# Optimization experiments

Measured on AMD Instinct MI355X. Metric: run time of the kernel, lower is better.

The kernel has to match this reference:

```python
import jax, jax.numpy as jnp
import numpy as np

B, C, D = 2, 2048, 1024   # batch, seq_len, hidden_size
I = 2048                  # intermediate_size (GLU hidden)
E, K = 8, 2               # n_experts, top_k
CF = 1.25                 # capacity factor


def setup_inputs() -> dict:
    key = jax.random.key(0)
    k1, k2, k3, k4 = jax.random.split(key, 4)
    scale = 0.02
    return {
        "hidden_states": jax.random.normal(k1, (B, C, D), jnp.float32),
        "Wg": jax.random.normal(k2, (E, D), jnp.float32) * scale,      # router gate weight [E, d]
        "W1": jax.random.normal(k3, (E, D, 2 * I), jnp.float32) * scale,  # expert in-proj
        "W2": jax.random.normal(k4, (E, I, D), jnp.float32) * scale,      # expert out-proj
    }


def reference(hidden_states, Wg, W1, W2):
    Bx, Cx, d = hidden_states.shape
    N = Bx * Cx
    cap = int(N * K * CF / E)  # exp_capacity (static)
    x = hidden_states.reshape(N, d)

    # --- router (eval mode: no noise) ---
    logits = x @ Wg.T                          # [N, E]
    top_v, top_i = jax.lax.top_k(logits, K)    # [N, K]
    gates = jax.nn.softmax(top_v, axis=-1)     # [N, K]

    # --- greedy capacity-limited assignment (token-major, then k), vectorized ---
    flat_e = top_i.reshape(N * K)              # expert id per (token, k) slot, in loop order
    gates_f = gates.reshape(N * K)
    tok = jnp.repeat(jnp.arange(N), K)         # token id per slot
    onehot = jax.nn.one_hot(flat_e, E, dtype=jnp.int32)
    pos = jnp.cumsum(onehot, axis=0) - 1       # running count per expert
    pos_f = jnp.take_along_axis(pos, flat_e[:, None], axis=1)[:, 0]
    keep = pos_f < cap                         # slots beyond capacity are dropped
    pos_safe = jnp.where(keep, pos_f, cap)     # out-of-range -> dropped by mode='drop'

    # --- dispatch: exp_batches[e, pos] = x[token] ---
    exp_batches = jnp.zeros((E, cap, d), x.dtype).at[flat_e, pos_safe].set(x[tok], mode='drop')

    # --- per-expert GLU MLP (batched over experts) ---
    h = jnp.einsum('ecd,edf->ecf', exp_batches, W1)       # [E, cap, 2I]
    inp, gate = jnp.split(h, 2, axis=-1)
    h = jax.nn.gelu(inp, approximate=False) * gate        # exact gelu, matches torch
    exp_out = jnp.einsum('eci,eid->ecd', h, W2)           # [E, cap, d]

    # --- combine: equals exp_mask.view(N,-1) @ exp_out.view(-1,d) ---
    gathered = exp_out[flat_e, jnp.minimum(pos_safe, cap - 1)]  # [N*K, d]
    contrib = jnp.where(keep, gates_f, 0.0)[:, None] * gathered
    out = jax.ops.segment_sum(contrib, tok, num_segments=N)    # [N, d]
    return out.reshape(Bx, Cx, d)
```

## Files before the change

kernel.cpp:

```cpp
#include <hip/hip_runtime.h>
#include <hip/hip_bf16.h>
#include <math.h>

#define N_TOK 4096
#define DIM   1024
#define NEXP  8
#define IDIM  2048
#define TWOI  4096
#define CAP   1280

#define W1_BLOCKS (64 * 16 * NEXP)
#define W2_BLOCKS (16 * 32 * NEXP)
#define ROUTER_BLOCKS (N_TOK / 4)

#define G1X 32
#define G1Y 10
#define G1_TRANS_Z ((W2_BLOCKS + G1X * G1Y - 1) / (G1X * G1Y))

using short8  = __attribute__((ext_vector_type(8))) short;
using floatx4 = __attribute__((ext_vector_type(4))) float;

__device__ __forceinline__ unsigned short f2b(float f) {
  __hip_bfloat16 h = __float2bfloat16(f);
  return *reinterpret_cast<unsigned short*>(&h);
}

__device__ __forceinline__ void async16(const unsigned short* g, unsigned short* l) {
  __builtin_amdgcn_global_load_lds(
      (const __attribute__((address_space(1))) unsigned int*)g,
      (__attribute__((address_space(3))) unsigned int*)l,
      16, 0, 0);
}

__device__ __forceinline__ void block_barrier() {
  __builtin_amdgcn_sched_barrier(0);
  asm volatile("" ::: "memory");
  __builtin_amdgcn_s_barrier();
  asm volatile("" ::: "memory");
  __builtin_amdgcn_sched_barrier(0);
}

__global__ __launch_bounds__(256) void prologue_kernel(const float* __restrict__ W1,
                                                       unsigned short* __restrict__ w1t,
                                                       const float* __restrict__ x,
                                                       const float* __restrict__ Wg,
                                                       unsigned short* __restrict__ xb,
                                                       int* __restrict__ top_i,
                                                       float* __restrict__ gates) {
  __shared__ __align__(16) float smem_f[NEXP * DIM];
  int bid = blockIdx.x;
  int tid = threadIdx.x;

  if (bid < W1_BLOCKS) {
    float (*tile)[65] = reinterpret_cast<float (*)[65]>(smem_f);
    int e = bid >> 10;
    int t = bid & 1023;
    const int R = DIM, C = TWOI;
    int r0 = (t & 15) * 64;
    int c0 = (t >> 4) * 64;
    const float* s = W1 + (size_t)e * R * C;
    unsigned short* d = w1t + (size_t)e * R * C;
    int tr = tid >> 4, tc = (tid & 15) * 4;
#pragma unroll
    for (int i = 0; i < 4; i++) {
      float4 v = *reinterpret_cast<const float4*>(&s[(size_t)(r0 + tr + i * 16) * C + c0 + tc]);
      tile[tr + i * 16][tc]     = v.x;
      tile[tr + i * 16][tc + 1] = v.y;
      tile[tr + i * 16][tc + 2] = v.z;
      tile[tr + i * 16][tc + 3] = v.w;
    }
    __syncthreads();
#pragma unroll
    for (int j = 0; j < 4; j++) {
      int c = (tid >> 4) + j * 16;
      int r4 = (tid & 15) * 4;
      ushort4 o;
      o.x = f2b(tile[r4][c]);
      o.y = f2b(tile[r4 + 1][c]);
      o.z = f2b(tile[r4 + 2][c]);
      o.w = f2b(tile[r4 + 3][c]);
      *reinterpret_cast<ushort4*>(&d[(size_t)(c0 + c) * R + r0 + r4]) = o;
    }
  } else {
    int rb = bid - W1_BLOCKS;
    float* wg = smem_f;
    for (int i = tid * 4; i < NEXP * DIM; i += 256 * 4) {
      *reinterpret_cast<float4*>(wg + i) = *reinterpret_cast<const float4*>(Wg + i);
    }
    __syncthreads();
    int wave = tid >> 6, lane = tid & 63;
    int t = rb * 4 + wave;
    const float* xr = x + (size_t)t * DIM;
    unsigned short* xbr = xb + (size_t)t * DIM;
    double acc[NEXP];
#pragma unroll
    for (int e = 0; e < NEXP; e++) acc[e] = 0.0;
    for (int i = lane; i < DIM; i += 64) {
      float xf = xr[i];
      xbr[i] = f2b(xf);
      double xv = (double)xf;
#pragma unroll
      for (int e = 0; e < NEXP; e++) acc[e] += xv * (double)wg[e * DIM + i];
    }
#pragma unroll
    for (int e = 0; e < NEXP; e++) {
#pragma unroll
      for (int m = 1; m < 64; m <<= 1) acc[e] += __shfl_xor(acc[e], m, 64);
    }
    if (lane == 0) {
      int i0 = 0; double v0 = acc[0];
      for (int e = 1; e < NEXP; e++) { if (acc[e] > v0) { v0 = acc[e]; i0 = e; } }
      int i1 = -1; double v1 = -1e300;
      for (int e = 0; e < NEXP; e++) { if (e != i0 && acc[e] > v1) { v1 = acc[e]; i1 = e; } }
      double e1 = exp(v1 - v0);
      float g0 = (float)(1.0 / (1.0 + e1));
      float g1 = (float)(e1 / (1.0 + e1));
      top_i[t * 2] = i0; top_i[t * 2 + 1] = i1;
      gates[t * 2] = g0; gates[t * 2 + 1] = g1;
    }
  }
}

__global__ __launch_bounds__(1024) void scan_kernel(const int* __restrict__ top_i,
                                                    const float* __restrict__ gates,
                                                    int* __restrict__ rowtok,
                                                    int* __restrict__ rowslot,
                                                    float* __restrict__ rowgate,
                                                    float* __restrict__ tokgate,
                                                    int* __restrict__ cnt) {
  __shared__ int hist[NEXP][1024];
  int t = threadIdx.x;
  int s0 = t * 8;
  int eloc[8];
  int c[NEXP];
#pragma unroll
  for (int e = 0; e < NEXP; e++) c[e] = 0;
#pragma unroll
  for (int j = 0; j < 8; j++) { int e = top_i[s0 + j]; eloc[j] = e; c[e]++; }
#pragma unroll
  for (int e = 0; e < NEXP; e++) hist[e][t] = c[e];
  __syncthreads();
  for (int step = 1; step < 1024; step <<= 1) {
    int tmp[NEXP];
#pragma unroll
    for (int e = 0; e < NEXP; e++) tmp[e] = (t >= step) ? hist[e][t - step] : 0;
    __syncthreads();
#pragma unroll
    for (int e = 0; e < NEXP; e++) hist[e][t] += tmp[e];
    __syncthreads();
  }
  int base[NEXP];
#pragma unroll
  for (int e = 0; e < NEXP; e++) base[e] = hist[e][t] - c[e];
  if (t < NEXP) {
    int tot = hist[t][1023];
    cnt[t] = tot < CAP ? tot : CAP;
  }
#pragma unroll
  for (int j = 0; j < 8; j++) {
    int s = s0 + j;
    int e = eloc[j];
    int pos = base[e]++;
    bool keep = pos < CAP;
    tokgate[s] = keep ? gates[s] : 0.0f;
    if (keep) {
      rowtok[e * CAP + pos]  = s >> 1;
      rowslot[e * CAP + pos] = s & 1;
      rowgate[e * CAP + pos] = gates[s];
    }
  }
}

__global__ __launch_bounds__(256, 2) void gemm1_kernel(const unsigned short* __restrict__ xb,
                                                       const unsigned short* __restrict__ w1t,
                                                       const int* __restrict__ rowtok,
                                                       const int* __restrict__ cnt,
                                                       unsigned short* __restrict__ H,
                                                       const float* __restrict__ W2,
                                                       unsigned short* __restrict__ w2t) {
  __shared__ __align__(16) unsigned char smem[65536];
  int tid  = threadIdx.x;
  int z = blockIdx.z;

  if (z >= NEXP) {
    int id = (z - NEXP) * (G1X * G1Y) + blockIdx.y * G1X + blockIdx.x;
    if (id >= W2_BLOCKS) return;
    float (*tile)[65] = reinterpret_cast<float (*)[65]>(smem);
    int e = id >> 9;
    int t = id & 511;
    const int R = IDIM, C = DIM;
    int r0 = (t & 31) * 64;
    int c0 = (t >> 5) * 64;
    const float* s = W2 + (size_t)e * R * C;
    unsigned short* d = w2t + (size_t)e * R * C;
    int tr = tid >> 4, tc = (tid & 15) * 4;
#pragma unroll
    for (int i = 0; i < 4; i++) {
      float4 v = *reinterpret_cast<const float4*>(&s[(size_t)(r0 + tr + i * 16) * C + c0 + tc]);
      tile[tr + i * 16][tc]     = v.x;
      tile[tr + i * 16][tc + 1] = v.y;
      tile[tr + i * 16][tc + 2] = v.z;
      tile[tr + i * 16][tc + 3] = v.w;
    }
    __syncthreads();
#pragma unroll
    for (int j = 0; j < 4; j++) {
      int c = (tid >> 4) + j * 16;
      int r4 = (tid & 15) * 4;
      ushort4 o;
      o.x = f2b(tile[r4][c]);
      o.y = f2b(tile[r4 + 1][c]);
      o.z = f2b(tile[r4 + 2][c]);
      o.w = f2b(tile[r4 + 3][c]);
      *reinterpret_cast<ushort4*>(&d[(size_t)(c0 + c) * R + r0 + r4]) = o;
    }
    return;
  }

  int e  = z;
  int m0 = blockIdx.y * 128;
  int i0 = blockIdx.x * 64;
  int cnte = cnt[e];
  if (m0 >= cnte) return;

  int lane = tid & 63;
  int wave = tid >> 6;

  int srA0 = wave * 32 + (lane >> 2);
  int srA1 = srA0 + 16;
  int srB  = wave * 16 + (lane >> 2);
  int sk   = (lane & 3) * 8;

  int ma0 = m0 + srA0, ma1 = m0 + srA1;
  int tok0 = (ma0 < cnte) ? rowtok[e * CAP + ma0] : 0;
  int tok1 = (ma1 < cnte) ? rowtok[e * CAP + ma1] : 0;

  const unsigned short* w1e = w1t + (size_t)e * TWOI * DIM;
  const unsigned short* gA0 = xb + (size_t)tok0 * DIM + sk;
  const unsigned short* gA1 = xb + (size_t)tok1 * DIM + sk;
  const unsigned short* gBi = w1e + (size_t)(i0 + srB) * DIM + sk;
  const unsigned short* gBg = w1e + (size_t)(i0 + srB + IDIM) * DIM + sk;

  int lane16 = lane & 15;
  int quad   = lane >> 4;
  int wm = (wave & 1) * 64;
  int wn = (wave >> 1) * 32;

  auto stage = [&](int s, int k0) {
#pragma unroll
    for (int b = 0; b < 2; b++) {
      int kk = k0 + b * 32;
      unsigned short* A  = (unsigned short*)(smem + s * 32768 + b * 8192);
      unsigned short* Bi = (unsigned short*)(smem + s * 32768 + 16384 + b * 4096);
      unsigned short* Bg = (unsigned short*)(smem + s * 32768 + 24576 + b * 4096);
      async16(gA0 + kk, A + (wave * 2 + 0) * 512);
      async16(gA1 + kk, A + (wave * 2 + 1) * 512);
      async16(gBi + kk, Bi + wave * 512);
      async16(gBg + kk, Bg + wave * 512);
    }
  };

  floatx4 acc_i[4][2], acc_g[4][2];
#pragma unroll
  for (int i = 0; i < 4; i++)
#pragma unroll
    for (int j = 0; j < 2; j++) {
      acc_i[i][j] = (floatx4){0.f, 0.f, 0.f, 0.f};
      acc_g[i][j] = (floatx4){0.f, 0.f, 0.f, 0.f};
    }

  const int T = DIM / 64;
  stage(0, 0);
  stage(1, 64);
  for (int t = 0; t < T; ++t) {
    if (t < T - 1) asm volatile("s_waitcnt vmcnt(8)" ::: "memory");
    else           asm volatile("s_waitcnt vmcnt(0)" ::: "memory");
    block_barrier();

    int s = t & 1;
#pragma unroll
    for (int b = 0; b < 2; b++) {
      const unsigned short* Ab  = (const unsigned short*)(smem + s * 32768 + b * 8192);
      const unsigned short* Bib = (const unsigned short*)(smem + s * 32768 + 16384 + b * 4096);
      const unsigned short* Bgb = (const unsigned short*)(smem + s * 32768 + 24576 + b * 4096);
      short8 a[4];
#pragma unroll
      for (int i = 0; i < 4; i++)
        a[i] = *(const short8*)&Ab[(wm + i * 16 + lane16) * 32 + quad * 8];
#pragma unroll
      for (int j = 0; j < 2; j++) {
        short8 bi = *(const short8*)&Bib[(wn + j * 16 + lane16) * 32 + quad * 8];
#pragma unroll
        for (int i = 0; i < 4; i++)
          acc_i[i][j] = __builtin_amdgcn_mfma_f32_16x16x32_bf16(a[i], bi, acc_i[i][j], 0, 0, 0);
        short8 bg = *(const short8*)&Bgb[(wn + j * 16 + lane16) * 32 + quad * 8];
#pragma unroll
        for (int i = 0; i < 4; i++)
          acc_g[i][j] = __builtin_amdgcn_mfma_f32_16x16x32_bf16(a[i], bg, acc_g[i][j], 0, 0, 0);
      }
    }

    block_barrier();
    if (t + 2 < T) stage(s, (t + 2) * 64);
  }

  unsigned short* He = H + (size_t)e * CAP * IDIM;
#pragma unroll
  for (int i = 0; i < 4; i++) {
#pragma unroll
    for (int r = 0; r < 4; r++) {
      int m = m0 + wm + i * 16 + quad * 4 + r;
#pragma unroll
      for (int j = 0; j < 2; j++) {
        int n = i0 + wn + j * 16 + lane16;
        float vi = acc_i[i][j][r];
        float vg = acc_g[i][j][r];
        float h = 0.5f * vi * (1.0f + erff(vi * 0.70710678118654752f)) * vg;
        He[(size_t)m * IDIM + n] = f2b(h);
      }
    }
  }
}

__global__ __launch_bounds__(256, 2) void gemm2_kernel(const unsigned short* __restrict__ H,
                                                       const unsigned short* __restrict__ w2t,
                                                       const int* __restrict__ cnt,
                                                       const int* __restrict__ rowtok,
                                                       const int* __restrict__ rowslot,
                                                       const float* __restrict__ rowgate,
                                                       float* __restrict__ out2) {
  int e  = blockIdx.z;
  int m0 = blockIdx.y * 128;
  int n0 = blockIdx.x * 128;
  int cnte = cnt[e];
  if (m0 >= cnte) return;

  __shared__ __align__(16) unsigned char smem[65536];

  int tid  = threadIdx.x;
  int lane = tid & 63;
  int wave = tid >> 6;

  int sr0 = wave * 32 + (lane >> 2);
  int sr1 = sr0 + 16;
  int sk  = (lane & 3) * 8;

  const unsigned short* He  = H + (size_t)e * CAP * IDIM;
  const unsigned short* w2e = w2t + (size_t)e * DIM * IDIM;
  const unsigned short* gA0 = He + (size_t)(m0 + sr0) * IDIM + sk;
  const unsigned short* gA1 = He + (size_t)(m0 + sr1) * IDIM + sk;
  const unsigned short* gB0 = w2e + (size_t)(n0 + sr0) * IDIM + sk;
  const unsigned short* gB1 = w2e + (size_t)(n0 + sr1) * IDIM + sk;

  int lane16 = lane & 15;
  int quad   = lane >> 4;
  int wm = (wave & 1) * 64;
  int wn = (wave >> 1) * 64;

  auto stage = [&](int s, int k0) {
#pragma unroll
    for (int b = 0; b < 2; b++) {
      int kk = k0 + b * 32;
      unsigned short* A = (unsigned short*)(smem + s * 32768 + b * 8192);
      unsigned short* B = (unsigned short*)(smem + s * 32768 + 16384 + b * 8192);
      async16(gA0 + kk, A + (wave * 2 + 0) * 512);
      async16(gA1 + kk, A + (wave * 2 + 1) * 512);
      async16(gB0 + kk, B + (wave * 2 + 0) * 512);
      async16(gB1 + kk, B + (wave * 2 + 1) * 512);
    }
  };

  floatx4 acc[4][4];
#pragma unroll
  for (int i = 0; i < 4; i++)
#pragma unroll
    for (int j = 0; j < 4; j++) acc[i][j] = (floatx4){0.f, 0.f, 0.f, 0.f};

  const int T = IDIM / 64;
  stage(0, 0);
  stage(1, 64);
  for (int t = 0; t < T; ++t) {
    if (t < T - 1) asm volatile("s_waitcnt vmcnt(8)" ::: "memory");
    else           asm volatile("s_waitcnt vmcnt(0)" ::: "memory");
    block_barrier();

    int s = t & 1;
#pragma unroll
    for (int b = 0; b < 2; b++) {
      const unsigned short* Ab = (const unsigned short*)(smem + s * 32768 + b * 8192);
      const unsigned short* Bb = (const unsigned short*)(smem + s * 32768 + 16384 + b * 8192);
      short8 a[4];
#pragma unroll
      for (int i = 0; i < 4; i++)
        a[i] = *(const short8*)&Ab[(wm + i * 16 + lane16) * 32 + quad * 8];
#pragma unroll
      for (int j = 0; j < 4; j++) {
        short8 bb = *(const short8*)&Bb[(wn + j * 16 + lane16) * 32 + quad * 8];
#pragma unroll
        for (int i = 0; i < 4; i++)
          acc[i][j] = __builtin_amdgcn_mfma_f32_16x16x32_bf16(a[i], bb, acc[i][j], 0, 0, 0);
      }
    }

    block_barrier();
    if (t + 2 < T) stage(s, (t + 2) * 64);
  }

#pragma unroll
  for (int i = 0; i < 4; i++) {
#pragma unroll
    for (int r = 0; r < 4; r++) {
      int m = m0 + wm + i * 16 + quad * 4 + r;
      if (m < cnte) {
        int tok = rowtok[e * CAP + m];
        int sl  = rowslot[e * CAP + m];
        float g = rowgate[e * CAP + m];
        float* orow = out2 + ((size_t)tok * 2 + sl) * DIM;
#pragma unroll
        for (int j = 0; j < 4; j++) {
          int n = n0 + wn + j * 16 + lane16;
          orow[n] = g * acc[i][j][r];
        }
      }
    }
  }
}

__global__ __launch_bounds__(256) void combine_kernel(const float* __restrict__ tokgate,
                                                      const float* __restrict__ out2,
                                                      float* __restrict__ out) {
  int t = blockIdx.x;
  int tid = threadIdx.x;
  float g0 = tokgate[t * 2], g1 = tokgate[t * 2 + 1];
  const float4* r0 = reinterpret_cast<const float4*>(out2 + (size_t)(t * 2) * DIM);
  const float4* r1 = reinterpret_cast<const float4*>(out2 + (size_t)(t * 2 + 1) * DIM);
  float4 a = r0[tid], b = r1[tid];
  float4 o;
  o.x = (g0 != 0.0f ? a.x : 0.0f) + (g1 != 0.0f ? b.x : 0.0f);
  o.y = (g0 != 0.0f ? a.y : 0.0f) + (g1 != 0.0f ? b.y : 0.0f);
  o.z = (g0 != 0.0f ? a.z : 0.0f) + (g1 != 0.0f ? b.z : 0.0f);
  o.w = (g0 != 0.0f ? a.w : 0.0f) + (g1 != 0.0f ? b.w : 0.0f);
  reinterpret_cast<float4*>(out + (size_t)t * DIM)[tid] = o;
}

extern "C" void kernel_launch(void* const* d_in, const int* in_sizes, int n_in,
                              void* d_out, int out_size, void* d_ws, size_t ws_size,
                              hipStream_t stream) {
  const float* x  = (const float*)d_in[0];
  const float* Wg = (const float*)d_in[1];
  const float* W1 = (const float*)d_in[2];
  const float* W2 = (const float*)d_in[3];
  float* out = (float*)d_out;

  char* ws = (char*)d_ws;
  size_t off = 0;
  auto alloc = [&](size_t bytes) -> void* {
    void* p = ws + off;
    off = (off + bytes + 255) & ~(size_t)255;
    return p;
  };
  int*   top_i   = (int*)alloc((size_t)N_TOK * 2 * sizeof(int));
  float* gates   = (float*)alloc((size_t)N_TOK * 2 * sizeof(float));
  int*   rowtok  = (int*)alloc((size_t)NEXP * CAP * sizeof(int));
  int*   rowslot = (int*)alloc((size_t)NEXP * CAP * sizeof(int));
  float* rowgate = (float*)alloc((size_t)NEXP * CAP * sizeof(float));
  float* tokgate = (float*)alloc((size_t)N_TOK * 2 * sizeof(float));
  int*   cnt     = (int*)alloc((size_t)NEXP * sizeof(int));
  unsigned short* xb  = (unsigned short*)alloc((size_t)N_TOK * DIM * 2);
  unsigned short* w1t = (unsigned short*)alloc((size_t)NEXP * TWOI * DIM * 2);
  unsigned short* w2t = (unsigned short*)alloc((size_t)NEXP * DIM * IDIM * 2);
  unsigned short* Hb  = (unsigned short*)alloc((size_t)NEXP * CAP * IDIM * 2);
  float* out2 = (float*)alloc((size_t)N_TOK * 2 * DIM * sizeof(float));
  if (off > ws_size) return;

  hipLaunchKernelGGL(prologue_kernel, dim3(W1_BLOCKS + ROUTER_BLOCKS), dim3(256), 0, stream,
                     W1, w1t, x, Wg, xb, top_i, gates);
  hipLaunchKernelGGL(scan_kernel, dim3(1), dim3(1024), 0, stream,
                     top_i, gates, rowtok, rowslot, rowgate, tokgate, cnt);
  hipLaunchKernelGGL(gemm1_kernel, dim3(G1X, G1Y, NEXP + G1_TRANS_Z), dim3(256), 0, stream,
                     xb, w1t, rowtok, cnt, Hb, W2, w2t);
  hipLaunchKernelGGL(gemm2_kernel, dim3(DIM / 128, CAP / 128, NEXP), dim3(256), 0, stream,
                     Hb, w2t, cnt, rowtok, rowslot, rowgate, out2);
  hipLaunchKernelGGL(combine_kernel, dim3(N_TOK), dim3(256), 0, stream,
                     tokgate, out2, out);
}
```

Baseline: 453.1 us.

## Enlarge gemm1 tile to 256x128 with 8 waves and 4-stage LDS pipeline

```diff
diff --git a/kernel.cpp b/kernel.cpp
--- a/kernel.cpp
+++ b/kernel.cpp
@@ -13,9 +13,9 @@
 #define W2_BLOCKS (16 * 32 * NEXP)
 #define ROUTER_BLOCKS (N_TOK / 4)
 
-#define G1X 32
-#define G1Y 10
-#define G1_TRANS_Z ((W2_BLOCKS + G1X * G1Y - 1) / (G1X * G1Y))
+#define G1X 16
+#define G1Y 5
+#define G1_TRANS_Z ((W2_BLOCKS / 2 + G1X * G1Y - 1) / (G1X * G1Y))
 
 using short8  = __attribute__((ext_vector_type(8))) short;
 using floatx4 = __attribute__((ext_vector_type(4))) float;
@@ -171,142 +171,157 @@
   }
 }
 
-__global__ __launch_bounds__(256, 2) void gemm1_kernel(const unsigned short* __restrict__ xb,
+__global__ __launch_bounds__(512, 1) void gemm1_kernel(const unsigned short* __restrict__ xb,
                                                        const unsigned short* __restrict__ w1t,
                                                        const int* __restrict__ rowtok,
                                                        const int* __restrict__ cnt,
                                                        unsigned short* __restrict__ H,
                                                        const float* __restrict__ W2,
                                                        unsigned short* __restrict__ w2t) {
-  __shared__ __align__(16) unsigned char smem[65536];
-  int tid  = threadIdx.x;
+  __shared__ __align__(16) unsigned char smem[131072];
+  int tid = threadIdx.x;
   int z = blockIdx.z;
 
   if (z >= NEXP) {
-    int id = (z - NEXP) * (G1X * G1Y) + blockIdx.y * G1X + blockIdx.x;
-    if (id >= W2_BLOCKS) return;
-    float (*tile)[65] = reinterpret_cast<float (*)[65]>(smem);
-    int e = id >> 9;
-    int t = id & 511;
-    const int R = IDIM, C = DIM;
-    int r0 = (t & 31) * 64;
-    int c0 = (t >> 5) * 64;
-    const float* s = W2 + (size_t)e * R * C;
-    unsigned short* d = w2t + (size_t)e * R * C;
-    int tr = tid >> 4, tc = (tid & 15) * 4;
-#pragma unroll
-    for (int i = 0; i < 4; i++) {
-      float4 v = *reinterpret_cast<const float4*>(&s[(size_t)(r0 + tr + i * 16) * C + c0 + tc]);
-      tile[tr + i * 16][tc]     = v.x;
-      tile[tr + i * 16][tc + 1] = v.y;
-      tile[tr + i * 16][tc + 2] = v.z;
-      tile[tr + i * 16][tc + 3] = v.w;
+    int slot = (z - NEXP) * (G1X * G1Y) + blockIdx.y * G1X + blockIdx.x;
+    int half = tid >> 8, t2 = tid & 255;
+    int id = slot * 2 + half;
+    bool valid = (id < W2_BLOCKS);
+    float* tile = (float*)smem + half * (64 * 65);
+    int tr = t2 >> 4, tc = (t2 & 15) * 4;
+    const float* s = nullptr;
+    unsigned short* d = nullptr;
+    int r0 = 0, c0 = 0;
+    if (valid) {
+      int e = id >> 9;
+      int t = id & 511;
+      r0 = (t & 31) * 64;
+      c0 = (t >> 5) * 64;
+      s = W2 + (size_t)e * IDIM * DIM;
+      d = w2t + (size_t)e * IDIM * DIM;
+#pragma unroll
+      for (int i = 0; i < 4; i++) {
+        float4 v = *reinterpret_cast<const float4*>(&s[(size_t)(r0 + tr + i * 16) * DIM + c0 + tc]);
+        tile[(tr + i * 16) * 65 + tc]     = v.x;
+        tile[(tr + i * 16) * 65 + tc + 1] = v.y;
+        tile[(tr + i * 16) * 65 + tc + 2] = v.z;
+        tile[(tr + i * 16) * 65 + tc + 3] = v.w;
+      }
     }
     __syncthreads();
-#pragma unroll
-    for (int j = 0; j < 4; j++) {
-      int c = (tid >> 4) + j * 16;
-      int r4 = (tid & 15) * 4;
-      ushort4 o;
-      o.x = f2b(tile[r4][c]);
-      o.y = f2b(tile[r4 + 1][c]);
-      o.z = f2b(tile[r4 + 2][c]);
-      o.w = f2b(tile[r4 + 3][c]);
-      *reinterpret_cast<ushort4*>(&d[(size_t)(c0 + c) * R + r0 + r4]) = o;
+    if (valid) {
+#pragma unroll
+      for (int j = 0; j < 4; j++) {
+        int c = (t2 >> 4) + j * 16;
+        int r4 = (t2 & 15) * 4;
+        ushort4 o;
+        o.x = f2b(tile[r4 * 65 + c]);
+        o.y = f2b(tile[(r4 + 1) * 65 + c]);
+        o.z = f2b(tile[(r4 + 2) * 65 + c]);
+        o.w = f2b(tile[(r4 + 3) * 65 + c]);
+        *reinterpret_cast<ushort4*>(&d[(size_t)(c0 + c) * IDIM + r0 + r4]) = o;
+      }
     }
     return;
   }
 
   int e  = z;
-  int m0 = blockIdx.y * 128;
-  int i0 = blockIdx.x * 64;
+  int m0 = blockIdx.y * 256;
+  int i0 = blockIdx.x * 128;
   int cnte = cnt[e];
   if (m0 >= cnte) return;
 
-  int lane = tid & 63;
-  int wave = tid >> 6;
-
-  int srA0 = wave * 32 + (lane >> 2);
-  int srA1 = srA0 + 16;
-  int srB  = wave * 16 + (lane >> 2);
-  int sk   = (lane & 3) * 8;
-
-  int ma0 = m0 + srA0, ma1 = m0 + srA1;
-  int tok0 = (ma0 < cnte) ? rowtok[e * CAP + ma0] : 0;
-  int tok1 = (ma1 < cnte) ? rowtok[e * CAP + ma1] : 0;
-
-  const unsigned short* w1e = w1t + (size_t)e * TWOI * DIM;
-  const unsigned short* gA0 = xb + (size_t)tok0 * DIM + sk;
-  const unsigned short* gA1 = xb + (size_t)tok1 * DIM + sk;
-  const unsigned short* gBi = w1e + (size_t)(i0 + srB) * DIM + sk;
-  const unsigned short* gBg = w1e + (size_t)(i0 + srB + IDIM) * DIM + sk;
-
-  int lane16 = lane & 15;
-  int quad   = lane >> 4;
-  int wm = (wave & 1) * 64;
+  unsigned short* sm = (unsigned short*)smem;
+  int lane = tid & 63, wave = tid >> 6;
+  int lane16 = lane & 15, quad = lane >> 4;
+  int wm = (wave & 1) * 128;
   int wn = (wave >> 1) * 32;
 
-  auto stage = [&](int s, int k0) {
-#pragma unroll
-    for (int b = 0; b < 2; b++) {
-      int kk = k0 + b * 32;
-      unsigned short* A  = (unsigned short*)(smem + s * 32768 + b * 8192);
-      unsigned short* Bi = (unsigned short*)(smem + s * 32768 + 16384 + b * 4096);
-      unsigned short* Bg = (unsigned short*)(smem + s * 32768 + 24576 + b * 4096);
-      async16(gA0 + kk, A + (wave * 2 + 0) * 512);
-      async16(gA1 + kk, A + (wave * 2 + 1) * 512);
-      async16(gBi + kk, Bi + wave * 512);
-      async16(gBg + kk, Bg + wave * 512);
-    }
+  int rA = tid >> 2;
+  int kq = (tid & 3) * 8;
+  int tokA0 = (m0 + rA       < cnte) ? rowtok[e * CAP + m0 + rA      ] : 0;
+  int tokA1 = (m0 + rA + 128 < cnte) ? rowtok[e * CAP + m0 + rA + 128] : 0;
+  const unsigned short* w1e  = w1t + (size_t)e * TWOI * DIM;
+  const unsigned short* gSA0 = xb + (size_t)tokA0 * DIM + kq;
+  const unsigned short* gSA1 = xb + (size_t)tokA1 * DIM + kq;
+  const unsigned short* gSBi = w1e + (size_t)(i0 + rA) * DIM + kq;
+  const unsigned short* gSBg = w1e + (size_t)(i0 + rA + IDIM) * DIM + kq;
+
+  auto stA = [&](int kt) {
+    unsigned short* base = sm + (kt & 3) * 16384 + wave * 512;
+    async16(gSA0 + kt * 32, base);
+    async16(gSA1 + kt * 32, base + 4096);
   };
-
-  floatx4 acc_i[4][2], acc_g[4][2];
-#pragma unroll
-  for (int i = 0; i < 4; i++)
+  auto stB = [&](int kt) {
+    unsigned short* base = sm + (kt & 3) * 16384 + 8192 + wave * 512;
+    async16(gSBi + kt * 32, base);
+    async16(gSBg + kt * 32, base + 4096);
+  };
+
+  floatx4 acc_i[8][2], acc_g[8][2];
+#pragma unroll
+  for (int i = 0; i < 8; i++)
 #pragma unroll
     for (int j = 0; j < 2; j++) {
       acc_i[i][j] = (floatx4){0.f, 0.f, 0.f, 0.f};
       acc_g[i][j] = (floatx4){0.f, 0.f, 0.f, 0.f};
     }
 
-  const int T = DIM / 64;
-  stage(0, 0);
-  stage(1, 64);
-  for (int t = 0; t < T; ++t) {
-    if (t < T - 1) asm volatile("s_waitcnt vmcnt(8)" ::: "memory");
-    else           asm volatile("s_waitcnt vmcnt(0)" ::: "memory");
+  stA(0); stB(0); stA(1); stB(1); stA(2); stB(2);
+  asm volatile("s_waitcnt vmcnt(8)" ::: "memory");
+  block_barrier();
+
+  const int NKT = DIM / 32;
+  for (int kt = 0; kt < NKT; ++kt) {
+    const unsigned short* Ab  = sm + (kt & 3) * 16384;
+    const unsigned short* Bib = Ab + 8192;
+    const unsigned short* Bgb = Ab + 12288;
+
+    short8 a[4], bi[2], bg[2];
+#pragma unroll
+    for (int i = 0; i < 4; i++)
+      a[i] = *(const short8*)&Ab[(wm + i * 16 + lane16) * 32 + quad * 8];
+#pragma unroll
+    for (int j = 0; j < 2; j++) {
+      bi[j] = *(const short8*)&Bib[(wn + j * 16 + lane16) * 32 + quad * 8];
+      bg[j] = *(const short8*)&Bgb[(wn + j * 16 + lane16) * 32 + quad * 8];
+    }
+    if (kt + 3 < NKT) stA(kt + 3);
     block_barrier();
-
-    int s = t & 1;
-#pragma unroll
-    for (int b = 0; b < 2; b++) {
-      const unsigned short* Ab  = (const unsigned short*)(smem + s * 32768 + b * 8192);
-      const unsigned short* Bib = (const unsigned short*)(smem + s * 32768 + 16384 + b * 4096);
-      const unsigned short* Bgb = (const unsigned short*)(smem + s * 32768 + 24576 + b * 4096);
-      short8 a[4];
-#pragma unroll
-      for (int i = 0; i < 4; i++)
-        a[i] = *(const short8*)&Ab[(wm + i * 16 + lane16) * 32 + quad * 8];
-#pragma unroll
-      for (int j = 0; j < 2; j++) {
-        short8 bi = *(const short8*)&Bib[(wn + j * 16 + lane16) * 32 + quad * 8];
-#pragma unroll
-        for (int i = 0; i < 4; i++)
-          acc_i[i][j] = __builtin_amdgcn_mfma_f32_16x16x32_bf16(a[i], bi, acc_i[i][j], 0, 0, 0);
-        short8 bg = *(const short8*)&Bgb[(wn + j * 16 + lane16) * 32 + quad * 8];
-#pragma unroll
-        for (int i = 0; i < 4; i++)
-          acc_g[i][j] = __builtin_amdgcn_mfma_f32_16x16x32_bf16(a[i], bg, acc_g[i][j], 0, 0, 0);
-      }
-    }
-
+    __builtin_amdgcn_s_setprio(1);
+#pragma unroll
+    for (int j = 0; j < 2; j++)
+#pragma unroll
+      for (int i = 0; i < 4; i++) {
+        acc_i[i][j] = __builtin_amdgcn_mfma_f32_16x16x32_bf16(a[i], bi[j], acc_i[i][j], 0, 0, 0);
+        acc_g[i][j] = __builtin_amdgcn_mfma_f32_16x16x32_bf16(a[i], bg[j], acc_g[i][j], 0, 0, 0);
+      }
+    __builtin_amdgcn_s_setprio(0);
     block_barrier();
-    if (t + 2 < T) stage(s, (t + 2) * 64);
+
+#pragma unroll
+    for (int i = 0; i < 4; i++)
+      a[i] = *(const short8*)&Ab[(wm + 64 + i * 16 + lane16) * 32 + quad * 8];
+    if (kt + 3 < NKT) stB(kt + 3);
+    block_barrier();
+    __builtin_amdgcn_s_setprio(1);
+#pragma unroll
+    for (int j = 0; j < 2; j++)
+#pragma unroll
+      for (int i = 0; i < 4; i++) {
+        acc_i[i + 4][j] = __builtin_amdgcn_mfma_f32_16x16x32_bf16(a[i], bi[j], acc_i[i + 4][j], 0, 0, 0);
+        acc_g[i + 4][j] = __builtin_amdgcn_mfma_f32_16x16x32_bf16(a[i], bg[j], acc_g[i + 4][j], 0, 0, 0);
+      }
+    __builtin_amdgcn_s_setprio(0);
+    if (kt <= NKT - 4)      { asm volatile("s_waitcnt vmcnt(8)" ::: "memory"); }
+    else if (kt == NKT - 3) { asm volatile("s_waitcnt vmcnt(4)" ::: "memory"); }
+    else if (kt == NKT - 2) { asm volatile("s_waitcnt vmcnt(0)" ::: "memory"); }
+    block_barrier();
   }
 
   unsigned short* He = H + (size_t)e * CAP * IDIM;
 #pragma unroll
-  for (int i = 0; i < 4; i++) {
+  for (int i = 0; i < 8; i++) {
 #pragma unroll
     for (int r = 0; r < 4; r++) {
       int m = m0 + wm + i * 16 + quad * 4 + r;
@@ -477,7 +492,7 @@
                      W1, w1t, x, Wg, xb, top_i, gates);
   hipLaunchKernelGGL(scan_kernel, dim3(1), dim3(1024), 0, stream,
                      top_i, gates, rowtok, rowslot, rowgate, tokgate, cnt);
-  hipLaunchKernelGGL(gemm1_kernel, dim3(G1X, G1Y, NEXP + G1_TRANS_Z), dim3(256), 0, stream,
+  hipLaunchKernelGGL(gemm1_kernel, dim3(G1X, G1Y, NEXP + G1_TRANS_Z), dim3(512), 0, stream,
                      xb, w1t, rowtok, cnt, Hb, W2, w2t);
   hipLaunchKernelGGL(gemm2_kernel, dim3(DIM / 128, CAP / 128, NEXP), dim3(256), 0, stream,
                      Hb, w2t, cnt, rowtok, rowslot, rowgate, out2);
```

Result: slower. 467.1 us (+3.1%).

## Drop double-buffered LDS pipeline for higher occupancy and swizzled block order

Applied to the files above, without the earlier changes.

```diff
diff --git a/kernel.cpp b/kernel.cpp
--- a/kernel.cpp
+++ b/kernel.cpp
@@ -30,14 +30,6 @@
       (const __attribute__((address_space(1))) unsigned int*)g,
       (__attribute__((address_space(3))) unsigned int*)l,
       16, 0, 0);
-}
-
-__device__ __forceinline__ void block_barrier() {
-  __builtin_amdgcn_sched_barrier(0);
-  asm volatile("" ::: "memory");
-  __builtin_amdgcn_s_barrier();
-  asm volatile("" ::: "memory");
-  __builtin_amdgcn_sched_barrier(0);
 }
 
 __global__ __launch_bounds__(256) void prologue_kernel(const float* __restrict__ W1,
@@ -171,14 +163,14 @@
   }
 }
 
-__global__ __launch_bounds__(256, 2) void gemm1_kernel(const unsigned short* __restrict__ xb,
+__global__ __launch_bounds__(256, 4) void gemm1_kernel(const unsigned short* __restrict__ xb,
                                                        const unsigned short* __restrict__ w1t,
                                                        const int* __restrict__ rowtok,
                                                        const int* __restrict__ cnt,
                                                        unsigned short* __restrict__ H,
                                                        const float* __restrict__ W2,
                                                        unsigned short* __restrict__ w2t) {
-  __shared__ __align__(16) unsigned char smem[65536];
+  __shared__ __align__(16) unsigned char smem[32768];
   int tid  = threadIdx.x;
   int z = blockIdx.z;
 
@@ -218,10 +210,16 @@
   }
 
   int e  = z;
-  int m0 = blockIdx.y * 128;
-  int i0 = blockIdx.x * 64;
+  int lin = blockIdx.y * G1X + blockIdx.x;
+  int swz = (lin & 7) * (G1X * G1Y / 8) + (lin >> 3);
+  int m0 = (swz / G1X) * 128;
+  int i0 = (swz % G1X) * 64;
   int cnte = cnt[e];
   if (m0 >= cnte) return;
+
+  unsigned short* As[2] = { (unsigned short*)smem,           (unsigned short*)(smem + 8192) };
+  unsigned short* Bi[2] = { (unsigned short*)(smem + 16384), (unsigned short*)(smem + 20480) };
+  unsigned short* Bg[2] = { (unsigned short*)(smem + 24576), (unsigned short*)(smem + 28672) };
 
   int lane = tid & 63;
   int wave = tid >> 6;
@@ -246,20 +244,6 @@
   int wm = (wave & 1) * 64;
   int wn = (wave >> 1) * 32;
 
-  auto stage = [&](int s, int k0) {
-#pragma unroll
-    for (int b = 0; b < 2; b++) {
-      int kk = k0 + b * 32;
-      unsigned short* A  = (unsigned short*)(smem + s * 32768 + b * 8192);
-      unsigned short* Bi = (unsigned short*)(smem + s * 32768 + 16384 + b * 4096);
-      unsigned short* Bg = (unsigned short*)(smem + s * 32768 + 24576 + b * 4096);
-      async16(gA0 + kk, A + (wave * 2 + 0) * 512);
-      async16(gA1 + kk, A + (wave * 2 + 1) * 512);
-      async16(gBi + kk, Bi + wave * 512);
-      async16(gBg + kk, Bg + wave * 512);
-    }
-  };
-
   floatx4 acc_i[4][2], acc_g[4][2];
 #pragma unroll
   for (int i = 0; i < 4; i++)
@@ -269,39 +253,36 @@
       acc_g[i][j] = (floatx4){0.f, 0.f, 0.f, 0.f};
     }
 
-  const int T = DIM / 64;
-  stage(0, 0);
-  stage(1, 64);
-  for (int t = 0; t < T; ++t) {
-    if (t < T - 1) asm volatile("s_waitcnt vmcnt(8)" ::: "memory");
-    else           asm volatile("s_waitcnt vmcnt(0)" ::: "memory");
-    block_barrier();
-
-    int s = t & 1;
+  for (int k0 = 0; k0 < DIM; k0 += 64) {
+    __syncthreads();
 #pragma unroll
     for (int b = 0; b < 2; b++) {
-      const unsigned short* Ab  = (const unsigned short*)(smem + s * 32768 + b * 8192);
-      const unsigned short* Bib = (const unsigned short*)(smem + s * 32768 + 16384 + b * 4096);
-      const unsigned short* Bgb = (const unsigned short*)(smem + s * 32768 + 24576 + b * 4096);
+      int kk = k0 + b * 32;
+      async16(gA0 + kk, As[b] + (wave * 2 + 0) * 512);
+      async16(gA1 + kk, As[b] + (wave * 2 + 1) * 512);
+      async16(gBi + kk, Bi[b] + wave * 512);
+      async16(gBg + kk, Bg[b] + wave * 512);
+    }
+    __syncthreads();
+
+#pragma unroll
+    for (int b = 0; b < 2; b++) {
       short8 a[4];
 #pragma unroll
       for (int i = 0; i < 4; i++)
-        a[i] = *(const short8*)&Ab[(wm + i * 16 + lane16) * 32 + quad * 8];
+        a[i] = *(const short8*)&As[b][(wm + i * 16 + lane16) * 32 + quad * 8];
 #pragma unroll
       for (int j = 0; j < 2; j++) {
-        short8 bi = *(const short8*)&Bib[(wn + j * 16 + lane16) * 32 + quad * 8];
+        short8 bi = *(const short8*)&Bi[b][(wn + j * 16 + lane16) * 32 + quad * 8];
 #pragma unroll
         for (int i = 0; i < 4; i++)
           acc_i[i][j] = __builtin_amdgcn_mfma_f32_16x16x32_bf16(a[i], bi, acc_i[i][j], 0, 0, 0);
-        short8 bg = *(const short8*)&Bgb[(wn + j * 16 + lane16) * 32 + quad * 8];
+        short8 bg = *(const short8*)&Bg[b][(wn + j * 16 + lane16) * 32 + quad * 8];
 #pragma unroll
         for (int i = 0; i < 4; i++)
           acc_g[i][j] = __builtin_amdgcn_mfma_f32_16x16x32_bf16(a[i], bg, acc_g[i][j], 0, 0, 0);
       }
     }
-
-    block_barrier();
-    if (t + 2 < T) stage(s, (t + 2) * 64);
   }
 
   unsigned short* He = H + (size_t)e * CAP * IDIM;
@@ -322,7 +303,7 @@
   }
 }
 
-__global__ __launch_bounds__(256, 2) void gemm2_kernel(const unsigned short* __restrict__ H,
+__global__ __launch_bounds__(256, 4) void gemm2_kernel(const unsigned short* __restrict__ H,
                                                        const unsigned short* __restrict__ w2t,
                                                        const int* __restrict__ cnt,
                                                        const int* __restrict__ rowtok,
@@ -330,12 +311,16 @@
                                                        const float* __restrict__ rowgate,
                                                        float* __restrict__ out2) {
   int e  = blockIdx.z;
-  int m0 = blockIdx.y * 128;
-  int n0 = blockIdx.x * 128;
+  int lin = blockIdx.y * 8 + blockIdx.x;
+  int swz = (lin & 7) * 10 + (lin >> 3);
+  int m0 = (swz / 8) * 128;
+  int n0 = (swz % 8) * 128;
   int cnte = cnt[e];
   if (m0 >= cnte) return;
 
-  __shared__ __align__(16) unsigned char smem[65536];
+  __shared__ __align__(16) unsigned char smem[32768];
+  unsigned short* As[2] = { (unsigned short*)smem,           (unsigned short*)(smem + 8192) };
+  unsigned short* Bs[2] = { (unsigned short*)(smem + 16384), (unsigned short*)(smem + 24576) };
 
   int tid  = threadIdx.x;
   int lane = tid & 63;
@@ -357,53 +342,38 @@
   int wm = (wave & 1) * 64;
   int wn = (wave >> 1) * 64;
 
-  auto stage = [&](int s, int k0) {
+  floatx4 acc[4][4];
+#pragma unroll
+  for (int i = 0; i < 4; i++)
+#pragma unroll
+    for (int j = 0; j < 4; j++) acc[i][j] = (floatx4){0.f, 0.f, 0.f, 0.f};
+
+  for (int k0 = 0; k0 < IDIM; k0 += 64) {
+    __syncthreads();
 #pragma unroll
     for (int b = 0; b < 2; b++) {
       int kk = k0 + b * 32;
-      unsigned short* A = (unsigned short*)(smem + s * 32768 + b * 8192);
-      unsigned short* B = (unsigned short*)(smem + s * 32768 + 16384 + b * 8192);
-      async16(gA0 + kk, A + (wave * 2 + 0) * 512);
-      async16(gA1 + kk, A + (wave * 2 + 1) * 512);
-      async16(gB0 + kk, B + (wave * 2 + 0) * 512);
-      async16(gB1 + kk, B + (wave * 2 + 1) * 512);
-    }
-  };
-
-  floatx4 acc[4][4];
-#pragma unroll
-  for (int i = 0; i < 4; i++)
-#pragma unroll
-    for (int j = 0; j < 4; j++) acc[i][j] = (floatx4){0.f, 0.f, 0.f, 0.f};
-
-  const int T = IDIM / 64;
-  stage(0, 0);
-  stage(1, 64);
-  for (int t = 0; t < T; ++t) {
-    if (t < T - 1) asm volatile("s_waitcnt vmcnt(8)" ::: "memory");
-    else           asm volatile("s_waitcnt vmcnt(0)" ::: "memory");
-    block_barrier();
-
-    int s = t & 1;
+      async16(gA0 + kk, As[b] + (wave * 2 + 0) * 512);
+      async16(gA1 + kk, As[b] + (wave * 2 + 1) * 512);
+      async16(gB0 + kk, Bs[b] + (wave * 2 + 0) * 512);
+      async16(gB1 + kk, Bs[b] + (wave * 2 + 1) * 512);
+    }
+    __syncthreads();
+
 #pragma unroll
     for (int b = 0; b < 2; b++) {
-      const unsigned short* Ab = (const unsigned short*)(smem + s * 32768 + b * 8192);
-      const unsigned short* Bb = (const unsigned short*)(smem + s * 32768 + 16384 + b * 8192);
       short8 a[4];
 #pragma unroll
       for (int i = 0; i < 4; i++)
-        a[i] = *(const short8*)&Ab[(wm + i * 16 + lane16) * 32 + quad * 8];
+        a[i] = *(const short8*)&As[b][(wm + i * 16 + lane16) * 32 + quad * 8];
 #pragma unroll
       for (int j = 0; j < 4; j++) {
-        short8 bb = *(const short8*)&Bb[(wn + j * 16 + lane16) * 32 + quad * 8];
+        short8 bb = *(const short8*)&Bs[b][(wn + j * 16 + lane16) * 32 + quad * 8];
 #pragma unroll
         for (int i = 0; i < 4; i++)
           acc[i][j] = __builtin_amdgcn_mfma_f32_16x16x32_bf16(a[i], bb, acc[i][j], 0, 0, 0);
       }
     }
-
-    block_barrier();
-    if (t + 2 < T) stage(s, (t + 2) * 64);
   }
 
 #pragma unroll
```

Measured after the change: 467.0 us. 1.03x slower.
